# Optimization experiments

Measured on AMD Instinct MI355X. Metric: run time of the kernel, lower is better.

## Reference

```python
import jax, jax.numpy as jnp
import numpy as np

DIM = 256
HEADS = 8


def setup_inputs() -> dict:
    key = jax.random.key(0)
    ks = jax.random.split(key, 12)
    B, N, L, C, H = 2, 1024, 4096, DIM, HEADS
    s = C ** -0.5
    inp = {
        "query": jax.random.normal(ks[0], (B, N, C), jnp.float32),
        "key": jax.random.normal(ks[1], (B, L, C), jnp.float32),
        "value": jax.random.normal(ks[2], (B, L, C), jnp.float32),
        "key_padding_mask": jnp.zeros((B, L), jnp.bool_),
        "hw_lvl": 1,
        # nn.Linear weights, stored as (out, in) like torch
        "Wq": jax.random.normal(ks[3], (C, C), jnp.float32) * s,
        "Wk": jax.random.normal(ks[4], (C, C), jnp.float32) * s,
        "Wv": jax.random.normal(ks[5], (C, C), jnp.float32) * s,
        "Wp": jax.random.normal(ks[6], (C, C), jnp.float32) * s,
        "bp": jax.random.normal(ks[7], (C,), jnp.float32) * 0.02,
        "W1": jax.random.normal(ks[8], (H, H), jnp.float32) * H ** -0.5,
        "b1": jax.random.normal(ks[9], (H,), jnp.float32) * 0.02,
        "W2": jax.random.normal(ks[10], (1, H), jnp.float32) * H ** -0.5,
        "b2": jax.random.normal(ks[11], (1,), jnp.float32) * 0.02,
    }
    return inp


def reference(query, key, value, key_padding_mask, hw_lvl,
              Wq, Wk, Wv, Wp, bp, W1, b1, W2, b2):
    # key_padding_mask and hw_lvl are accepted but unused by the original module.
    B, N, C = query.shape
    L = key.shape[1]
    H = W1.shape[0]
    D = C // H
    scale = D ** -0.5

    q = (query @ Wq.T).reshape(B, N, H, D)  # bnhd
    k = (key @ Wk.T).reshape(B, L, H, D)    # blhd
    v = (value @ Wv.T).reshape(B, L, H, D)  # blhd

    # raw attention scores [B, H, N, L]
    attn = jnp.einsum("bnhd,blhd->bhnl", q, k) * scale

    # per-score tiny MLP over the head axis -> mask [B, N, L, 1]
    scores_nlh = attn.transpose(0, 2, 3, 1)  # [B, N, L, H]
    new_feats = jax.nn.relu(scores_nlh @ W1.T + b1)
    mask = jax.nn.relu(new_feats @ W2.T + b2)  # [B, N, L, 1]

    a = jax.nn.softmax(attn, axis=-1)  # dropout p=0 -> identity
    x = jnp.einsum("bhnl,blhd->bnhd", a, v).reshape(B, N, C)
    x = x @ Wp.T + bp
    return x, mask
```

## Files before the change

### kernel.cpp

```cpp
#include <hip/hip_runtime.h>

typedef unsigned short u16;
typedef unsigned int u32;
typedef __attribute__((ext_vector_type(8))) short bf16x8;
typedef __attribute__((ext_vector_type(4))) short bf16x4;
typedef __attribute__((ext_vector_type(4))) float f32x4;

#define QK_SCALE 0.17677669529663687f

__device__ inline float bf2f(u16 h) {
    u32 u = ((u32)h) << 16; float f; __builtin_memcpy(&f, &u, 4); return f;
}
__device__ inline u16 f2bf(float f) {
    u32 u; __builtin_memcpy(&u, &f, 4);
    u = u + 0x7fffu + ((u >> 16) & 1u);
    return (u16)(u >> 16);
}

__global__ __launch_bounds__(256) void cvt_all_kernel(
    const float* __restrict__ q, const float* __restrict__ k,
    const float* __restrict__ v,
    const float* __restrict__ Wq, const float* __restrict__ Wk,
    const float* __restrict__ Wv, const float* __restrict__ Wp,
    u16* __restrict__ qf, u16* __restrict__ kf, u16* __restrict__ vf,
    u16* __restrict__ wqb, u16* __restrict__ wkb, u16* __restrict__ wvb,
    u16* __restrict__ wpb)
{
    const int bx = blockIdx.x;
    const float* src; u16* dst; int base;
    if (bx < 256)       { src = q;  dst = qf;  base = bx; }
    else if (bx < 1280) { src = k;  dst = kf;  base = bx - 256; }
    else if (bx < 2304) { src = v;  dst = vf;  base = bx - 1280; }
    else if (bx < 2336) { src = Wq; dst = wqb; base = bx - 2304; }
    else if (bx < 2368) { src = Wk; dst = wkb; base = bx - 2336; }
    else if (bx < 2400) { src = Wv; dst = wvb; base = bx - 2368; }
    else                { src = Wp; dst = wpb; base = bx - 2400; }
    const int i = base * 2048 + threadIdx.x * 8;
    const f32x4 a = *(const f32x4*)(src + i);
    const f32x4 b = *(const f32x4*)(src + i + 4);
    bf16x8 o;
#pragma unroll
    for (int j = 0; j < 4; ++j) {
        o[j]     = (short)f2bf(a[j]);
        o[j + 4] = (short)f2bf(b[j]);
    }
    *(bf16x8*)(dst + i) = o;
}

__global__ __launch_bounds__(256) void proj_kernel(
    const u16* __restrict__ qf, const u16* __restrict__ kf,
    const u16* __restrict__ vf,
    const u16* __restrict__ wqb, const u16* __restrict__ wkb,
    const u16* __restrict__ wvb,
    u16* __restrict__ qb, u16* __restrict__ kb, u16* __restrict__ vt)
{
    const int bx = blockIdx.x;
    const u16 *X, *W; u16* outb; int m0, mode;
    if (bx < 128)      { X = qf; W = wqb; outb = qb; m0 = bx * 16; mode = 2; }
    else if (bx < 640) { X = kf; W = wkb; outb = kb; m0 = (bx - 128) * 16; mode = 0; }
    else               { X = vf; W = wvb; outb = vt; m0 = (bx - 640) * 16; mode = 1; }

    const int lane = threadIdx.x & 63;
    const int w = threadIdx.x >> 6;
    const int r = lane & 15, g = lane >> 4;
    const int c0 = blockIdx.y * 64 + w * 16;
    const u16* ap = X + (long)(m0 + r) * 256 + g * 8;
    const u16* bp = W + (long)(c0 + r) * 256 + g * 8;

    bf16x8 af[8], bf[8];
#pragma unroll
    for (int ks = 0; ks < 8; ++ks) af[ks] = *(const bf16x8*)(ap + ks * 32);
#pragma unroll
    for (int ks = 0; ks < 8; ++ks) bf[ks] = *(const bf16x8*)(bp + ks * 32);

    f32x4 acc = {0.f, 0.f, 0.f, 0.f};
#pragma unroll
    for (int ks = 0; ks < 8; ++ks)
        acc = __builtin_amdgcn_mfma_f32_16x16x32_bf16(af[ks], bf[ks], acc, 0, 0, 0);

    const int c = c0 + r;
    if (mode == 1) {
        const int m_ = m0 + g * 4;
        const int b = m_ >> 12, l = m_ & 4095;
        bf16x4 pk;
#pragma unroll
        for (int j = 0; j < 4; ++j) pk[j] = (short)f2bf(acc[j]);
        *(bf16x4*)(vt + (long)b * 1048576 + (long)(l >> 2) * 1024 + c * 4) = pk;
    } else {
#pragma unroll
        for (int j = 0; j < 4; ++j) {
            const int m = m0 + g * 4 + j;
            if (mode == 2) outb[(long)m * 256 + c] = f2bf(acc[j] * QK_SCALE);
            else           outb[(long)m * 256 + c] = f2bf(acc[j]);
        }
    }
}

__global__ __launch_bounds__(256, 2) void attn_split_kernel(
    const u16* __restrict__ qb, const u16* __restrict__ kb,
    const u16* __restrict__ vt,
    const float* __restrict__ W1, const float* __restrict__ b1,
    const float* __restrict__ W2, const float* __restrict__ b2,
    u16* __restrict__ Opart, float* __restrict__ stats,
    float* __restrict__ out)
{
    __shared__ float ored[4][8][2][2][16][4];
    __shared__ float rs[4][8][16];

    const int tid = threadIdx.x;
    const int w = tid >> 6, lane = tid & 63;
    const int r = lane & 15, g = lane >> 4;
    const int bi = blockIdx.y;
    const int n0 = blockIdx.x * 16;
    const int cz = blockIdx.z;

    float w1r[64], b1r[8], w2r[8];
#pragma unroll
    for (int i = 0; i < 64; ++i) w1r[i] = W1[i];
#pragma unroll
    for (int i = 0; i < 8; ++i) { b1r[i] = b1[i]; w2r[i] = W2[i]; }
    const float b2r = b2[0];

    bf16x8 qh[8];
    const long qbase = (long)(bi * 1024 + n0 + r) * 256 + g * 8;
#pragma unroll
    for (int h = 0; h < 8; ++h)
        qh[h] = *(const bf16x8*)(qb + qbase + h * 32);

    f32x4 oacc[8][2];
#pragma unroll
    for (int h = 0; h < 8; ++h)
#pragma unroll
        for (int c = 0; c < 2; ++c) oacc[h][c] = (f32x4){0.f, 0.f, 0.f, 0.f};
    float rsum[8];
#pragma unroll
    for (int h = 0; h < 8; ++h) rsum[h] = 0.f;

    bf16x8 kf[8];
    {
        const long kbb = (long)(bi * 4096 + cz * 512 + w * 16 + r) * 256 + g * 8;
#pragma unroll
        for (int h = 0; h < 8; ++h)
            kf[h] = *(const bf16x8*)(kb + kbb + h * 32);
    }

    for (int t = 0; t < 8; ++t) {
        const int l0 = cz * 512 + t * 64;

        f32x4 ss[8];
#pragma unroll
        for (int h = 0; h < 8; ++h) {
            f32x4 z = {0.f, 0.f, 0.f, 0.f};
            ss[h] = __builtin_amdgcn_mfma_f32_16x16x32_bf16(kf[h], qh[h], z, 0, 0, 0);
        }

        if (t < 7) {
            const long kbb = (long)(bi * 4096 + l0 + 64 + w * 16 + r) * 256 + g * 8;
#pragma unroll
            for (int h = 0; h < 8; ++h)
                kf[h] = *(const bf16x8*)(kb + kbb + h * 32);
        }

        {
            f32x4 mv4;
#pragma unroll
            for (int j = 0; j < 4; ++j) {
                float mv = b2r;
#pragma unroll
                for (int f = 0; f < 8; ++f) {
                    float ft = b1r[f];
#pragma unroll
                    for (int h = 0; h < 8; ++h)
                        ft = fmaf(ss[h][j], w1r[f * 8 + h], ft);
                    mv = fmaf(fmaxf(ft, 0.f), w2r[f], mv);
                }
                mv4[j] = fmaxf(mv, 0.f);
            }
            *(f32x4*)(out + 524288l + (long)(bi * 1024 + n0 + r) * 4096
                      + l0 + w * 16 + g * 4) = mv4;
        }

        bf16x4 vf[8][2];
        {
            const u16* vb = vt + (long)bi * 1048576 +
                            (long)((l0 >> 2) + w * 4 + g) * 1024;
#pragma unroll
            for (int h = 0; h < 8; ++h)
#pragma unroll
                for (int c = 0; c < 2; ++c)
                    vf[h][c] = *(const bf16x4*)(vb + (h * 32 + c * 16 + r) * 4);
        }

        bf16x4 pa[8];
#pragma unroll
        for (int h = 0; h < 8; ++h) {
            float e0 = __expf(ss[h][0] - 8.f);
            float e1 = __expf(ss[h][1] - 8.f);
            float e2 = __expf(ss[h][2] - 8.f);
            float e3 = __expf(ss[h][3] - 8.f);
            rsum[h] += (e0 + e1) + (e2 + e3);
            u32 u0, u1, u2, u3;
            __builtin_memcpy(&u0, &e0, 4); __builtin_memcpy(&u1, &e1, 4);
            __builtin_memcpy(&u2, &e2, 4); __builtin_memcpy(&u3, &e3, 4);
            u32 lohi[2];
            lohi[0] = (u0 >> 16) | (u1 & 0xFFFF0000u);
            lohi[1] = (u2 >> 16) | (u3 & 0xFFFF0000u);
            __builtin_memcpy(&pa[h], lohi, 8);
        }

#pragma unroll
        for (int h = 0; h < 8; ++h)
#pragma unroll
            for (int c = 0; c < 2; ++c)
                oacc[h][c] = __builtin_amdgcn_mfma_f32_16x16x16bf16_1k(
                    pa[h], vf[h][c], oacc[h][c], 0, 0, 0);
    }

#pragma unroll
    for (int h = 0; h < 8; ++h) {
        float v = rsum[h];
        v += __shfl_xor(v, 16);
        v += __shfl_xor(v, 32);
        if (g == 0) rs[w][h][r] = v;
    }
#pragma unroll
    for (int ph = 0; ph < 2; ++ph) {
        if ((g >> 1) == ph) {
#pragma unroll
            for (int h = 0; h < 8; ++h)
#pragma unroll
                for (int c = 0; c < 2; ++c)
                    *(f32x4*)&ored[w][h][c][g & 1][r][0] = oacc[h][c];
        }
        __syncthreads();
        if (ph == 0 && tid < 128) {
            const int h = tid >> 4, n = tid & 15;
            stats[((long)(bi * 8 + cz) * 8 + h) * 1024 + n0 + n] =
                rs[0][h][n] + rs[1][h][n] + rs[2][h][n] + rs[3][h][n];
        }
        {
            const int h = tid >> 5, c = (tid >> 4) & 1, rr = tid & 15;
#pragma unroll
            for (int g2 = 0; g2 < 2; ++g2)
#pragma unroll
                for (int j = 0; j < 4; ++j) {
                    const float val =
                        ored[0][h][c][g2][rr][j] + ored[1][h][c][g2][rr][j] +
                        ored[2][h][c][g2][rr][j] + ored[3][h][c][g2][rr][j];
                    const int n = (ph * 2 + g2) * 4 + j;
                    Opart[((long)(bi * 8 + cz) * 1024 + n0 + n) * 256
                          + h * 32 + c * 16 + rr] = f2bf(val);
                }
        }
        if (ph == 0) __syncthreads();
    }
}

__global__ __launch_bounds__(256) void reduce_kernel(
    const u16* __restrict__ Opart, const float* __restrict__ stats,
    const u16* __restrict__ wpb, const float* __restrict__ bp,
    float* __restrict__ out)
{
    __shared__ __align__(16) u16 xt[16 * 272];
    const int tid = threadIdx.x;
    const int w = tid >> 6, lane = tid & 63;
    const int r = lane & 15, g = lane >> 4;
    const int bi = blockIdx.y, n0 = blockIdx.x * 16;
    const int n = tid >> 4, cg = tid & 15, h = cg >> 1;

    float S = 0.f, O[16];
#pragma unroll
    for (int k = 0; k < 16; ++k) O[k] = 0.f;
#pragma unroll
    for (int c = 0; c < 8; ++c) {
        S += stats[((long)(bi * 8 + c) * 8 + h) * 1024 + n0 + n];
        const bf16x8* op = (const bf16x8*)(Opart +
            ((long)(bi * 8 + c) * 1024 + n0 + n) * 256 + cg * 16);
        bf16x8 v0 = op[0], v1 = op[1];
#pragma unroll
        for (int k = 0; k < 8; ++k) {
            O[k]     += bf2f((u16)v0[k]);
            O[k + 8] += bf2f((u16)v1[k]);
        }
    }
    const float inv = 1.f / S;
#pragma unroll
    for (int k = 0; k < 16; ++k)
        xt[n * 272 + cg * 16 + k] = f2bf(O[k] * inv);
    __syncthreads();

    bf16x8 a8[8];
#pragma unroll
    for (int ks = 0; ks < 8; ++ks)
        a8[ks] = *(const bf16x8*)(&xt[r * 272 + ks * 32 + g * 8]);
#pragma unroll
    for (int kblk = 0; kblk < 4; ++kblk) {
        const int cp0 = (w + kblk * 4) * 16;
        f32x4 acc = {0.f, 0.f, 0.f, 0.f};
#pragma unroll
        for (int ks = 0; ks < 8; ++ks) {
            bf16x8 wb = *(const bf16x8*)(wpb + (long)(cp0 + r) * 256 + ks * 32 + g * 8);
            acc = __builtin_amdgcn_mfma_f32_16x16x32_bf16(a8[ks], wb, acc, 0, 0, 0);
        }
        const int cp = cp0 + r;
        const float bpv = bp[cp];
#pragma unroll
        for (int j = 0; j < 4; ++j) {
            const int nn = g * 4 + j;
            out[(long)(bi * 1024 + n0 + nn) * 256 + cp] = acc[j] + bpv;
        }
    }
}

extern "C" void kernel_launch(void* const* d_in, const int* in_sizes, int n_in,
                              void* d_out, int out_size, void* d_ws, size_t ws_size,
                              hipStream_t stream)
{
    const float* query = (const float*)d_in[0];
    const float* key   = (const float*)d_in[1];
    const float* value = (const float*)d_in[2];
    const float* Wq = (const float*)d_in[5];
    const float* Wk = (const float*)d_in[6];
    const float* Wv = (const float*)d_in[7];
    const float* Wp = (const float*)d_in[8];
    const float* bp = (const float*)d_in[9];
    const float* W1 = (const float*)d_in[10];
    const float* b1 = (const float*)d_in[11];
    const float* W2 = (const float*)d_in[12];
    const float* b2 = (const float*)d_in[13];

    u16* qb    = (u16*)d_ws;
    u16* kb    = qb + 524288;
    u16* vtp   = kb + 2097152;
    u16* wpb   = vtp + 2097152;
    u16* Opart = wpb + 65536;
    u16* kfb   = Opart;
    u16* vfb   = Opart + 2097152;
    float* stats = (float*)(Opart + 4194304);
    u16* qfb   = (u16*)(stats + 131072);
    u16* wqb   = qfb + 524288;
    u16* wkb   = wqb + 65536;
    u16* wvb   = wkb + 65536;
    float* out = (float*)d_out;

    cvt_all_kernel<<<2432, 256, 0, stream>>>(
        query, key, value, Wq, Wk, Wv, Wp,
        qfb, kfb, vfb, wqb, wkb, wvb, wpb);
    proj_kernel<<<dim3(1152, 4), 256, 0, stream>>>(
        qfb, kfb, vfb, wqb, wkb, wvb, qb, kb, vtp);
    attn_split_kernel<<<dim3(64, 2, 8), 256, 0, stream>>>(
        qb, kb, vtp, W1, b1, W2, b2, Opart, stats, out);
    reduce_kernel<<<dim3(64, 2), 256, 0, stream>>>(Opart, stats, wpb, bp, out);
}
```

Before: 114.6 us.

## Software-pipeline QK MFMA one tile ahead with double-buffered score registers

Fully unrolls the 8-step L loop and double-buffers the score registers. The QK MFMA for the next tile is issued while the current tile's gating MLP, exp and PV MFMA run, and K loads are prefetched two tiles ahead. The aim is to overlap matrix-core latency and global-load latency with the VALU-heavy mask MLP and softmax work. In exchange it raises register pressure, from a second 8x f32x4 score buffer plus full unrolling, which could lower occupancy or cause spills.

```diff
diff --git a/kernel.cpp b/kernel.cpp
--- a/kernel.cpp
+++ b/kernel.cpp
@@ -137,84 +137,91 @@
     for (int h = 0; h < 8; ++h) rsum[h] = 0.f;
 
     bf16x8 kf[8];
-    {
-        const long kbb = (long)(bi * 4096 + cz * 512 + w * 16 + r) * 256 + g * 8;
-#pragma unroll
-        for (int h = 0; h < 8; ++h)
-            kf[h] = *(const bf16x8*)(kb + kbb + h * 32);
-    }
-
-    for (int t = 0; t < 8; ++t) {
-        const int l0 = cz * 512 + t * 64;
-
-        f32x4 ss[8];
-#pragma unroll
-        for (int h = 0; h < 8; ++h) {
-            f32x4 z = {0.f, 0.f, 0.f, 0.f};
-            ss[h] = __builtin_amdgcn_mfma_f32_16x16x32_bf16(kf[h], qh[h], z, 0, 0, 0);
-        }
-
-        if (t < 7) {
-            const long kbb = (long)(bi * 4096 + l0 + 64 + w * 16 + r) * 256 + g * 8;
-#pragma unroll
-            for (int h = 0; h < 8; ++h)
-                kf[h] = *(const bf16x8*)(kb + kbb + h * 32);
-        }
-
-        {
-            f32x4 mv4;
-#pragma unroll
-            for (int j = 0; j < 4; ++j) {
-                float mv = b2r;
-#pragma unroll
-                for (int f = 0; f < 8; ++f) {
-                    float ft = b1r[f];
-#pragma unroll
-                    for (int h = 0; h < 8; ++h)
-                        ft = fmaf(ss[h][j], w1r[f * 8 + h], ft);
-                    mv = fmaf(fmaxf(ft, 0.f), w2r[f], mv);
-                }
-                mv4[j] = fmaxf(mv, 0.f);
-            }
-            *(f32x4*)(out + 524288l + (long)(bi * 1024 + n0 + r) * 4096
-                      + l0 + w * 16 + g * 4) = mv4;
-        }
-
-        bf16x4 vf[8][2];
-        {
-            const u16* vb = vt + (long)bi * 1048576 +
-                            (long)((l0 >> 2) + w * 4 + g) * 1024;
-#pragma unroll
-            for (int h = 0; h < 8; ++h)
-#pragma unroll
-                for (int c = 0; c < 2; ++c)
-                    vf[h][c] = *(const bf16x4*)(vb + (h * 32 + c * 16 + r) * 4);
-        }
-
-        bf16x4 pa[8];
-#pragma unroll
-        for (int h = 0; h < 8; ++h) {
-            float e0 = __expf(ss[h][0] - 8.f);
-            float e1 = __expf(ss[h][1] - 8.f);
-            float e2 = __expf(ss[h][2] - 8.f);
-            float e3 = __expf(ss[h][3] - 8.f);
-            rsum[h] += (e0 + e1) + (e2 + e3);
-            u32 u0, u1, u2, u3;
-            __builtin_memcpy(&u0, &e0, 4); __builtin_memcpy(&u1, &e1, 4);
-            __builtin_memcpy(&u2, &e2, 4); __builtin_memcpy(&u3, &e3, 4);
-            u32 lohi[2];
-            lohi[0] = (u0 >> 16) | (u1 & 0xFFFF0000u);
-            lohi[1] = (u2 >> 16) | (u3 & 0xFFFF0000u);
-            __builtin_memcpy(&pa[h], lohi, 8);
-        }
-
-#pragma unroll
-        for (int h = 0; h < 8; ++h)
-#pragma unroll
-            for (int c = 0; c < 2; ++c)
-                oacc[h][c] = __builtin_amdgcn_mfma_f32_16x16x16bf16_1k(
-                    pa[h], vf[h][c], oacc[h][c], 0, 0, 0);
-    }
+    f32x4 ssA[8], ssB[8];
+
+#define LOADK(TT) { \
+    const long kbb = (long)(bi * 4096 + cz * 512 + (TT) * 64 + w * 16 + r) * 256 + g * 8; \
+    _Pragma("unroll") \
+    for (int h = 0; h < 8; ++h) kf[h] = *(const bf16x8*)(kb + kbb + h * 32); }
+
+#define QKSTEP(DST) { \
+    _Pragma("unroll") \
+    for (int h = 0; h < 8; ++h) { \
+        f32x4 z = {0.f, 0.f, 0.f, 0.f}; \
+        DST[h] = __builtin_amdgcn_mfma_f32_16x16x32_bf16(kf[h], qh[h], z, 0, 0, 0); } }
+
+    LOADK(0);
+    QKSTEP(ssA);
+    LOADK(1);
+
+#define BODY(T, SC, SN) { \
+    const int l0 = cz * 512 + (T) * 64; \
+     \
+    bf16x4 vf[8][2]; \
+    { \
+        const u16* vb = vt + (long)bi * 1048576 + (long)((l0 >> 2) + w * 4 + g) * 1024; \
+        _Pragma("unroll") \
+        for (int h = 0; h < 8; ++h) \
+            _Pragma("unroll") \
+            for (int c = 0; c < 2; ++c) \
+                vf[h][c] = *(const bf16x4*)(vb + (h * 32 + c * 16 + r) * 4); \
+    } \
+     \
+    if ((T) < 7) QKSTEP(SN); \
+    if ((T) < 6) LOADK((T) + 2); \
+     \
+    { \
+        f32x4 mv4; \
+        _Pragma("unroll") \
+        for (int j = 0; j < 4; ++j) { \
+            float mv = b2r; \
+            _Pragma("unroll") \
+            for (int f = 0; f < 8; ++f) { \
+                float ft = b1r[f]; \
+                _Pragma("unroll") \
+                for (int h = 0; h < 8; ++h) \
+                    ft = fmaf(SC[h][j], w1r[f * 8 + h], ft); \
+                mv = fmaf(fmaxf(ft, 0.f), w2r[f], mv); \
+            } \
+            mv4[j] = fmaxf(mv, 0.f); \
+        } \
+        *(f32x4*)(out + 524288l + (long)(bi * 1024 + n0 + r) * 4096 \
+                  + l0 + w * 16 + g * 4) = mv4; \
+    } \
+     \
+    { \
+        bf16x4 pa[8]; \
+        _Pragma("unroll") \
+        for (int h = 0; h < 8; ++h) { \
+            float e0 = __expf(SC[h][0] - 8.f); \
+            float e1 = __expf(SC[h][1] - 8.f); \
+            float e2 = __expf(SC[h][2] - 8.f); \
+            float e3 = __expf(SC[h][3] - 8.f); \
+            rsum[h] += (e0 + e1) + (e2 + e3); \
+            u32 u0, u1, u2, u3; \
+            __builtin_memcpy(&u0, &e0, 4); __builtin_memcpy(&u1, &e1, 4); \
+            __builtin_memcpy(&u2, &e2, 4); __builtin_memcpy(&u3, &e3, 4); \
+            u32 lohi[2]; \
+            lohi[0] = (u0 >> 16) | (u1 & 0xFFFF0000u); \
+            lohi[1] = (u2 >> 16) | (u3 & 0xFFFF0000u); \
+            __builtin_memcpy(&pa[h], lohi, 8); \
+        } \
+        _Pragma("unroll") \
+        for (int h = 0; h < 8; ++h) \
+            _Pragma("unroll") \
+            for (int c = 0; c < 2; ++c) \
+                oacc[h][c] = __builtin_amdgcn_mfma_f32_16x16x16bf16_1k( \
+                    pa[h], vf[h][c], oacc[h][c], 0, 0, 0); \
+    } }
+
+    BODY(0, ssA, ssB); BODY(1, ssB, ssA);
+    BODY(2, ssA, ssB); BODY(3, ssB, ssA);
+    BODY(4, ssA, ssB); BODY(5, ssB, ssA);
+    BODY(6, ssA, ssB); BODY(7, ssB, ssA);
+
+#undef BODY
+#undef QKSTEP
+#undef LOADK
 
 #pragma unroll
     for (int h = 0; h < 8; ++h) {
```

Result: slower. 208.6 us (+81.9%).
